# Performance work log

Measured on AMD Instinct MI355X. Metric: run time of the kernel, lower is better.

Reference implementation:

```python
import math
import jax, jax.numpy as jnp
import numpy as np

D_MODEL = 1024
NHEAD = 16
HEAD_DIM = D_MODEL // NHEAD
BATCH = 2
SEQ = 2048


def setup_inputs() -> dict:
    key = jax.random.key(0)
    ks = jax.random.split(key, 8)
    data = jax.random.normal(ks[0], (BATCH, SEQ, D_MODEL), dtype=jnp.float32)
    temporal = jax.random.uniform(ks[1], (BATCH, SEQ), dtype=jnp.float32)
    mask = jnp.zeros((SEQ, SEQ), dtype=jnp.float32)
    s = 1.0 / math.sqrt(D_MODEL)
    Wq = jax.random.normal(ks[2], (D_MODEL, D_MODEL), dtype=jnp.float32) * s
    Wk = jax.random.normal(ks[3], (D_MODEL, D_MODEL), dtype=jnp.float32) * s
    Wv = jax.random.normal(ks[4], (D_MODEL, D_MODEL), dtype=jnp.float32) * s
    bq = jax.random.normal(ks[5], (D_MODEL,), dtype=jnp.float32) * 0.02
    bk = jax.random.normal(ks[6], (D_MODEL,), dtype=jnp.float32) * 0.02
    bv = jax.random.normal(ks[7], (D_MODEL,), dtype=jnp.float32) * 0.02
    return {"data": data, "temporal": temporal, "mask": mask,
            "Wq": Wq, "bq": bq, "Wk": Wk, "bk": bk, "Wv": Wv, "bv": bv}


def _rotate_half_pairs(x):
    # x: [..., s] with s even; pairs (x0,x1) -> (-x1, x0) interleaved
    x2 = x.reshape(x.shape[:-1] + (-1, 2))  # [..., s//2, 2]
    rot = jnp.stack([-x2[..., 1], x2[..., 0]], axis=-1)
    return rot.reshape(x.shape)


def reference(data, temporal, mask, Wq, bq, Wk, bk, Wv, bv):
    B, L, D = data.shape
    H, S = NHEAD, HEAD_DIM
    scale = math.sqrt(S)

    query = (data @ Wq + bq).reshape(B, L, H, S)
    key_ = (data @ Wk + bk).reshape(B, L, H, S)
    value = (data @ Wv + bv).reshape(B, L, H, S)

    # freq = 10000^(-arange(0, S, 2)/S), repeat_interleave(2) -> [S]
    freq = jnp.power(10000.0, -jnp.arange(0, S, 2, dtype=jnp.float32) / S)
    freq = jnp.repeat(freq, 2)
    freqs = temporal[:, :, None] * freq[None, None, :]  # [B, L, S]
    cosine = jnp.cos(freqs)[:, :, None, :]  # [B, L, 1, S]
    sine = jnp.sin(freqs)[:, :, None, :]

    rq = query * cosine + _rotate_half_pairs(query) * sine
    rk = key_ * cosine + _rotate_half_pairs(key_) * sine

    logits = jnp.einsum('bqhs,bkhs->bhqk', rq, rk) / scale
    logits = logits + mask  # mask: [L, L], broadcasts over b,h
    weights = jax.nn.softmax(logits, axis=-1)
    context = jnp.einsum('bhqk,bkhs->bqhs', weights, value)
    return context.reshape(B, L, D)
```

## Files before the change

### kernel.cpp

```cpp
#include <hip/hip_runtime.h>
#include <hip/hip_bf16.h>

#define D_MODEL 1024
#define NHEAD   16
#define HEAD_DIM 64
#define BATCH   2
#define SEQ     2048
#define NTOK    (BATCH*SEQ)

#define FREQ_LOG2 0.20762050593046015f

typedef short  bfrag __attribute__((ext_vector_type(8)));
typedef float  ffrag __attribute__((ext_vector_type(4)));

__device__ inline ushort f2bf(float x) {
    __hip_bfloat16 h = __float2bfloat16(x);
    return __builtin_bit_cast(ushort, h);
}
__device__ inline float bf2f(ushort u) {
    return __builtin_bit_cast(float, (uint)u << 16);
}
__device__ inline void split_bf(float x, ushort& hi, ushort& lo) {
    __hip_bfloat16 h = __float2bfloat16(x);
    hi = __builtin_bit_cast(ushort, h);
    lo = f2bf(x - __bfloat162float(h));
}

__device__ inline void gload16(const ushort* g, ushort* l) {
    __builtin_amdgcn_global_load_lds(
        (const __attribute__((address_space(1))) void*)g,
        (__attribute__((address_space(3))) void*)l, 16, 0, 0);
}

__device__ inline void barrier_lds_only() {
    asm volatile("s_waitcnt lgkmcnt(0)\n\ts_barrier" ::: "memory");
}

__device__ inline void barrier_vm4() {
    asm volatile("s_waitcnt vmcnt(4) lgkmcnt(0)\n\ts_barrier" ::: "memory");
}

__device__ inline void barrier_vm8() {
    asm volatile("s_waitcnt vmcnt(8) lgkmcnt(0)\n\ts_barrier" ::: "memory");
}

__global__ __launch_bounds__(256)
void prep(const float* __restrict__ data, ushort* __restrict__ Ahi,
          ushort* __restrict__ Alo,
          const float* __restrict__ mask, ushort* __restrict__ Mbf,
          int* __restrict__ MZnz,
          const float* __restrict__ Wq, const float* __restrict__ Wk,
          const float* __restrict__ Wv, ushort* __restrict__ WThi,
          const float* __restrict__ temporal, float* __restrict__ cst)
{
    __shared__ float T[64][65];
    __shared__ int bnz;
    const int bid = blockIdx.x, t = threadIdx.x;

    if (bid < 4096) {
        const int i4 = (bid * 256 + t) * 4;
        const float4 v = *(const float4*)(data + i4);
        ushort4 h, l;
        split_bf(v.x, h.x, l.x); split_bf(v.y, h.y, l.y);
        split_bf(v.z, h.z, l.z); split_bf(v.w, h.w, l.w);
        *(ushort4*)(Ahi + i4) = h;
        *(ushort4*)(Alo + i4) = l;
        return;
    }
    if (bid < 8192) {
        const int mi = bid - 4096;
        const int i4 = (mi * 256 + t) * 4;
        const float4 v = *(const float4*)(mask + i4);
        ushort4 h;
        h.x = f2bf(v.x); h.y = f2bf(v.y); h.z = f2bf(v.z); h.w = f2bf(v.w);
        *(ushort4*)(Mbf + i4) = h;
        const int nz = (v.x != 0.f) || (v.y != 0.f) || (v.z != 0.f) || (v.w != 0.f);
        if (t == 0) bnz = 0;
        __syncthreads();
        if (nz) atomicOr(&bnz, 1);
        __syncthreads();
        if (t == 0) MZnz[mi] = bnz;
        return;
    }
    if (bid < 8960) {
        const int id  = bid - 8192;
        const int z   = id >> 8;
        const int rem = id & 255;
        const int k0  = (rem & 15) * 64, n0 = (rem >> 4) * 64;
        const float* W = (z == 0) ? Wq : (z == 1) ? Wk : Wv;
        ushort* thi = WThi + (size_t)z * D_MODEL * D_MODEL;

        #pragma unroll
        for (int i = 0; i < 4; i++) {
            const int f = i * 256 + t, r = f >> 4, c = (f & 15) * 4;
            const float4 v = *(const float4*)(W + (size_t)(k0 + r) * D_MODEL + n0 + c);
            T[r][c] = v.x; T[r][c + 1] = v.y; T[r][c + 2] = v.z; T[r][c + 3] = v.w;
        }
        __syncthreads();
        #pragma unroll
        for (int i = 0; i < 4; i++) {
            const int f = i * 256 + t, nr = f >> 4, kc = (f & 15) * 4;
            ushort4 h;
            h.x = f2bf(T[kc + 0][nr]);
            h.y = f2bf(T[kc + 1][nr]);
            h.z = f2bf(T[kc + 2][nr]);
            h.w = f2bf(T[kc + 3][nr]);
            const size_t o = (size_t)(n0 + nr) * D_MODEL + k0 + kc;
            *(ushort4*)(thi + o) = h;
        }
        return;
    }
    const int id3 = bid - 8960;
    const int m   = id3 * 8 + (t >> 5);
    const int j   = t & 31;
    const float tv = temporal[m];
    const float fr = exp2f(-(float)(2 * j) * FREQ_LOG2);
    float s, c;
    __sincosf(tv * fr, &s, &c);
    *(float2*)(cst + (size_t)m * 64 + 2 * j) = make_float2(c, s);
}

#define BK 32

union GemmSM {
    ushort st[3][2][128 * BK];
    float  c[64 * 132];
};

__global__ __launch_bounds__(256, 3)
void gemm_qkv(const ushort* __restrict__ Ahi, const ushort* __restrict__ Alo,
              const ushort* __restrict__ WThi,
              const float* __restrict__ bq, const float* __restrict__ bk,
              const float* __restrict__ bv, const float* __restrict__ cst,
              const int* __restrict__ MZnz, int* __restrict__ Flag,
              ushort* __restrict__ Qhi, ushort* __restrict__ Qlo,
              ushort* __restrict__ Khi,
              ushort* __restrict__ VT)
{
    __shared__ GemmSM sm;
    __shared__ int flg;
    const int bidl = blockIdx.x;
    const int xcd  = bidl & 7, kk = bidl >> 3;
    const int m0   = (xcd * 4 + (kk & 3)) * 128;
    const int nz   = kk >> 2;
    const int n0   = (nz & 7) * 128;
    const int z    = nz >> 3;

    const int t = threadIdx.x;

    if (bidl == 0) {
        if (t == 0) flg = 0;
        __syncthreads();
        int acc = 0;
        const int4* z4 = (const int4*)MZnz;
        #pragma unroll
        for (int i = 0; i < 4; i++) {
            const int4 v = z4[t * 4 + i];
            acc |= v.x | v.y | v.z | v.w;
        }
        if (acc) atomicOr(&flg, 1);
        __syncthreads();
        if (t == 0) Flag[0] = flg;
    }

    const float* bias = (z == 0) ? bq : (z == 1) ? bk : bv;
    const ushort* Bh = WThi + (size_t)z * D_MODEL * D_MODEL;

    const int w = t >> 6, lane = t & 63;
    const int lane15 = lane & 15, quad8 = (lane >> 4) * 8, quad = lane >> 4;
    const int wm = (w >> 1) * 64, wn = (w & 1) * 64;

    ffrag acc[4][4];
    #pragma unroll
    for (int i = 0; i < 4; i++)
        #pragma unroll
        for (int j = 0; j < 4; j++) acc[i][j] = (ffrag){0.f, 0.f, 0.f, 0.f};

    const int wr = w * 32;
    const int lr = lane >> 2;
    const int lc = (((lane & 3) ^ ((lane >> 3) & 3))) * 8;

    auto stage = [&](int bsel, int k0) {
        #pragma unroll
        for (int ch = 0; ch < 2; ch++) {
            const int rb = wr + ch * 16;
            const ushort* ga = Ahi + (size_t)(m0 + rb + lr) * D_MODEL + k0 + lc;
            const ushort* gb = Bh  + (size_t)(n0 + rb + lr) * D_MODEL + k0 + lc;
            gload16(ga, &sm.st[bsel][0][rb * BK]);
            gload16(gb, &sm.st[bsel][1][rb * BK]);
        }
    };

    bfrag alp0, alp1, alp2, alp3;
    {
        alp0 = *(const bfrag*)(Alo + (size_t)(m0 + wm +  0 + lane15) * D_MODEL + quad8);
        alp1 = *(const bfrag*)(Alo + (size_t)(m0 + wm + 16 + lane15) * D_MODEL + quad8);
        alp2 = *(const bfrag*)(Alo + (size_t)(m0 + wm + 32 + lane15) * D_MODEL + quad8);
        alp3 = *(const bfrag*)(Alo + (size_t)(m0 + wm + 48 + lane15) * D_MODEL + quad8);
    }

    stage(0, 0);
    stage(1, BK);
    barrier_vm4();

    const int rdsw = (quad ^ ((lane15 >> 1) & 3)) * 8;

    int cur = 0;
    for (int i = 0; i < 32; i++) {
        const int k0 = i * BK;
        const int st2 = (cur >= 1) ? cur - 1 : 2;
        stage(st2, k0 + 2 * BK);

        bfrag al0 = alp0, al1 = alp1, al2 = alp2, al3 = alp3;
        {
            const int kn = k0 + BK;
            alp0 = *(const bfrag*)(Alo + (size_t)(m0 + wm +  0 + lane15) * D_MODEL + kn + quad8);
            alp1 = *(const bfrag*)(Alo + (size_t)(m0 + wm + 16 + lane15) * D_MODEL + kn + quad8);
            alp2 = *(const bfrag*)(Alo + (size_t)(m0 + wm + 32 + lane15) * D_MODEL + kn + quad8);
            alp3 = *(const bfrag*)(Alo + (size_t)(m0 + wm + 48 + lane15) * D_MODEL + kn + quad8);
        }

        bfrag ah[4];
        #pragma unroll
        for (int mt = 0; mt < 4; mt++)
            ah[mt] = *(const bfrag*)&sm.st[cur][0][(wm + mt * 16 + lane15) * BK + rdsw];

        #pragma unroll
        for (int nt = 0; nt < 4; nt++) {
            const bfrag bh = *(const bfrag*)&sm.st[cur][1][(wn + nt * 16 + lane15) * BK + rdsw];
            {
                ffrag a = acc[0][nt];
                a = __builtin_amdgcn_mfma_f32_16x16x32_bf16(ah[0], bh, a, 0, 0, 0);
                a = __builtin_amdgcn_mfma_f32_16x16x32_bf16(al0,   bh, a, 0, 0, 0);
                acc[0][nt] = a;
            }
            {
                ffrag a = acc[1][nt];
                a = __builtin_amdgcn_mfma_f32_16x16x32_bf16(ah[1], bh, a, 0, 0, 0);
                a = __builtin_amdgcn_mfma_f32_16x16x32_bf16(al1,   bh, a, 0, 0, 0);
                acc[1][nt] = a;
            }
            {
                ffrag a = acc[2][nt];
                a = __builtin_amdgcn_mfma_f32_16x16x32_bf16(ah[2], bh, a, 0, 0, 0);
                a = __builtin_amdgcn_mfma_f32_16x16x32_bf16(al2,   bh, a, 0, 0, 0);
                acc[2][nt] = a;
            }
            {
                ffrag a = acc[3][nt];
                a = __builtin_amdgcn_mfma_f32_16x16x32_bf16(ah[3], bh, a, 0, 0, 0);
                a = __builtin_amdgcn_mfma_f32_16x16x32_bf16(al3,   bh, a, 0, 0, 0);
                acc[3][nt] = a;
            }
        }
        barrier_vm8();
        cur = (cur == 2) ? 0 : cur + 1;
    }

    float bn[4];
    #pragma unroll
    for (int nt = 0; nt < 4; nt++) bn[nt] = bias[n0 + wn + nt * 16 + lane15];

    const int CST = (z == 2) ? 129 : 132;

    #pragma unroll
    for (int p = 0; p < 2; p++) {
        if (p) __syncthreads();
        if ((w >> 1) == p) {
            #pragma unroll
            for (int mt = 0; mt < 4; mt++)
                #pragma unroll
                for (int nt = 0; nt < 4; nt++)
                    #pragma unroll
                    for (int rr = 0; rr < 4; rr++)
                        sm.c[(mt * 16 + quad * 4 + rr) * CST + wn + nt * 16 + lane15] =
                            acc[mt][nt][rr] + bn[nt];
        }
        __syncthreads();

        if (z < 2) {
            ushort* ohi = (z == 0) ? Qhi : Khi;
            const float sc = (z == 0) ? 0.125f : 1.0f;
            #pragma unroll
            for (int i = 0; i < 8; i++) {
                const int f = i * 256 + t, r = f >> 5, c4 = (f & 31) * 4;
                float4 v = *(float4*)&sm.c[r * 132 + c4];
                const int m = m0 + p * 64 + r;
                const float4 cs4 = *(const float4*)(cst + (size_t)m * 64 + (c4 & 63));
                const float c0 = cs4.x, s0 = cs4.y, c1v = cs4.z, s1 = cs4.w;
                const float y0 = (v.x * c0 - v.y * s0) * sc;
                const float y1 = (v.y * c0 + v.x * s0) * sc;
                const float y2 = (v.z * c1v - v.w * s1) * sc;
                const float y3 = (v.w * c1v + v.z * s1) * sc;
                ushort4 h, l;
                split_bf(y0, h.x, l.x); split_bf(y1, h.y, l.y);
                split_bf(y2, h.z, l.z); split_bf(y3, h.w, l.w);
                const size_t o = (size_t)m * D_MODEL + n0 + c4;
                *(ushort4*)(ohi + o) = h;
                if (z == 0) *(ushort4*)(Qlo + o) = l;
            }
        } else {
            const int bb = m0 >> 11;
            #pragma unroll
            for (int i = 0; i < 4; i++) {
                const int cid = i * 256 + t, col = cid >> 3, tg = (cid & 7) * 8;
                ushort u8[8];
                #pragma unroll
                for (int j = 0; j < 8; j++) u8[j] = f2bf(sm.c[(tg + j) * 129 + col]);
                const int ncol = n0 + col, hh = ncol >> 6, d = ncol & 63;
                const size_t dst = ((size_t)(bb * NHEAD + hh) * HEAD_DIM + d) * SEQ +
                                   (m0 & (SEQ - 1)) + p * 64 + tg;
                *(int4*)(VT + dst) = *(int4*)u8;
            }
        }
    }
}

__global__ __launch_bounds__(256, 2)
void attn_mfma(const ushort* __restrict__ Qhi, const ushort* __restrict__ Qlo,
               const ushort* __restrict__ Khi,
               const ushort* __restrict__ VT,  const ushort* __restrict__ maskbf,
               const int* __restrict__ Flag,
               float* __restrict__ out)
{
    __shared__ ushort lsK[2][128 * 64], lsV[2][64 * 128], lsP[128 * 64];

    const int bid  = blockIdx.x;
    const int bh   = (bid & 7) * 4 + (bid >> 7);
    const int qb   = (bid >> 3) & 15;
    const int b    = bh >> 4, h = bh & 15;
    const int q0   = qb * 128;

    const int t = threadIdx.x, w = t >> 6, lane = t & 63;
    const int lane15 = lane & 15, quad = lane >> 4;
    const size_t tok0 = (size_t)b * SEQ;

    const int mz = Flag[0];

    bfrag qh[2][2], ql[2][2];
    #pragma unroll
    for (int su = 0; su < 2; su++) {
        const size_t qrow = (tok0 + q0 + w * 32 + su * 16 + lane15) * D_MODEL +
                            h * HEAD_DIM;
        #pragma unroll
        for (int ks = 0; ks < 2; ks++) {
            qh[su][ks] = *(const bfrag*)(Qhi + qrow + ks * 32 + quad * 8);
            ql[su][ks] = *(const bfrag*)(Qlo + qrow + ks * 32 + quad * 8);
        }
    }

    const short one_bf = (short)0x3F80;
    const bfrag ones = {one_bf, one_bf, one_bf, one_bf,
                        one_bf, one_bf, one_bf, one_bf};

    ffrag of[2][4], of_l[2];
    #pragma unroll
    for (int su = 0; su < 2; su++) {
        of_l[su] = (ffrag){0.f, 0.f, 0.f, 0.f};
        #pragma unroll
        for (int nt = 0; nt < 4; nt++)
            of[su][nt] = (ffrag){0.f, 0.f, 0.f, 0.f};
    }

    const int rK  = t >> 3, cK = (t & 7) * 8;
    const int swK = ((t & 7) ^ (rK & 7)) * 8;
    const int rV   = t >> 2;
    const int keyV = ((rV & 3) << 2) | ((rV >> 2) & 3);
    const ushort* Kh0 = Khi + tok0 * D_MODEL + h * HEAD_DIM;
    const ushort* Vt0 = VT + (size_t)(b * NHEAD + h) * HEAD_DIM * SEQ;

    const size_t kof0 = (size_t)(rK +  0) * D_MODEL + cK;
    const size_t kof1 = (size_t)(rK + 32) * D_MODEL + cK;
    const size_t kof2 = (size_t)(rK + 64) * D_MODEL + cK;
    const size_t kof3 = (size_t)(rK + 96) * D_MODEL + cK;
    const size_t vof  = (size_t)rV * SEQ + (t & 3) * 8;

    int4 pk0 = *(const int4*)(Kh0 + kof0);
    int4 pk1 = *(const int4*)(Kh0 + kof1);
    int4 pk2 = *(const int4*)(Kh0 + kof2);
    int4 pk3 = *(const int4*)(Kh0 + kof3);
    int4 pv0 = *(const int4*)(Vt0 + vof +  0);
    int4 pv1 = *(const int4*)(Vt0 + vof + 32);
    int4 pv2 = *(const int4*)(Vt0 + vof + 64);
    int4 pv3 = *(const int4*)(Vt0 + vof + 96);

    *(int4*)&lsK[0][(rK +  0) * 64 + swK] = pk0;
    *(int4*)&lsK[0][(rK + 32) * 64 + swK] = pk1;
    *(int4*)&lsK[0][(rK + 64) * 64 + swK] = pk2;
    *(int4*)&lsK[0][(rK + 96) * 64 + swK] = pk3;
    *(int4*)&lsV[0][rV * 128 + (((t & 3) +  0) ^ keyV) * 8] = pv0;
    *(int4*)&lsV[0][rV * 128 + (((t & 3) +  4) ^ keyV) * 8] = pv1;
    *(int4*)&lsV[0][rV * 128 + (((t & 3) +  8) ^ keyV) * 8] = pv2;
    *(int4*)&lsV[0][rV * 128 + (((t & 3) + 12) ^ keyV) * 8] = pv3;

    pk0 = *(const int4*)(Kh0 + 128 * D_MODEL + kof0);
    pk1 = *(const int4*)(Kh0 + 128 * D_MODEL + kof1);
    pk2 = *(const int4*)(Kh0 + 128 * D_MODEL + kof2);
    pk3 = *(const int4*)(Kh0 + 128 * D_MODEL + kof3);
    pv0 = *(const int4*)(Vt0 + 128 + vof +  0);
    pv1 = *(const int4*)(Vt0 + 128 + vof + 32);
    pv2 = *(const int4*)(Vt0 + 128 + vof + 64);
    pv3 = *(const int4*)(Vt0 + 128 + vof + 96);
    barrier_lds_only();

    const ushort* mrow0 = maskbf + (size_t)(q0 + w * 32 + quad * 4) * SEQ;
    const ushort* mrow1 = maskbf + (size_t)(q0 + w * 32 + 16 + quad * 4) * SEQ;

    const int krd  = lane15 & 7;
    const int keyr = (((lane15 >> 2) & 3) << 1) | (lane15 & 1);
    const int keyVr = ((lane15 & 3) << 2) | ((lane15 >> 2) & 3);

    int cur = 0;
    for (int kt = 0; kt < SEQ; kt += 128) {
        if (kt + 128 < SEQ) {
            *(int4*)&lsK[cur ^ 1][(rK +  0) * 64 + swK] = pk0;
            *(int4*)&lsK[cur ^ 1][(rK + 32) * 64 + swK] = pk1;
            *(int4*)&lsK[cur ^ 1][(rK + 64) * 64 + swK] = pk2;
            *(int4*)&lsK[cur ^ 1][(rK + 96) * 64 + swK] = pk3;
            *(int4*)&lsV[cur ^ 1][rV * 128 + (((t & 3) +  0) ^ keyV) * 8] = pv0;
            *(int4*)&lsV[cur ^ 1][rV * 128 + (((t & 3) +  4) ^ keyV) * 8] = pv1;
            *(int4*)&lsV[cur ^ 1][rV * 128 + (((t & 3) +  8) ^ keyV) * 8] = pv2;
            *(int4*)&lsV[cur ^ 1][rV * 128 + (((t & 3) + 12) ^ keyV) * 8] = pv3;
        }

        const int ktn = (kt + 256 < SEQ) ? kt + 256 : 0;
        const ushort* KhT = Kh0 + (size_t)ktn * D_MODEL;
        const ushort* VtT = Vt0 + ktn;
        pk0 = *(const int4*)(KhT + kof0);
        pk1 = *(const int4*)(KhT + kof1);
        pk2 = *(const int4*)(KhT + kof2);
        pk3 = *(const int4*)(KhT + kof3);
        pv0 = *(const int4*)(VtT + vof +  0);
        pv1 = *(const int4*)(VtT + vof + 32);
        pv2 = *(const int4*)(VtT + vof + 64);
        pv3 = *(const int4*)(VtT + vof + 96);

        #pragma unroll
        for (int half = 0; half < 2; half++) {
            const int kb = kt + half * 64;

            float mv0[4][4], mv1[4][4];
            if (mz) {
                #pragma unroll
                for (int nt = 0; nt < 4; nt++)
                    #pragma unroll
                    for (int rr = 0; rr < 4; rr++) {
                        mv0[nt][rr] = bf2f(mrow0[(size_t)rr * SEQ + kb + nt * 16 + lane15]);
                        mv1[nt][rr] = bf2f(mrow1[(size_t)rr * SEQ + kb + nt * 16 + lane15]);
                    }
            }

            ffrag s0[4], s1[4];
            __builtin_amdgcn_s_setprio(1);
            #pragma unroll
            for (int nt = 0; nt < 4; nt++) {
                const int krow = half * 64 + nt * 16 + lane15;
                const bfrag kf0 = *(const bfrag*)&lsK[cur][krow * 64 + ((0 + quad) ^ krd) * 8];
                const bfrag kf1 = *(const bfrag*)&lsK[cur][krow * 64 + ((4 + quad) ^ krd) * 8];
                ffrag a0 = (ffrag){0.f, 0.f, 0.f, 0.f};
                ffrag a1 = (ffrag){0.f, 0.f, 0.f, 0.f};
                a0 = __builtin_amdgcn_mfma_f32_16x16x32_bf16(qh[0][0], kf0, a0, 0, 0, 0);
                a0 = __builtin_amdgcn_mfma_f32_16x16x32_bf16(ql[0][0], kf0, a0, 0, 0, 0);
                a0 = __builtin_amdgcn_mfma_f32_16x16x32_bf16(qh[0][1], kf1, a0, 0, 0, 0);
                a0 = __builtin_amdgcn_mfma_f32_16x16x32_bf16(ql[0][1], kf1, a0, 0, 0, 0);
                a1 = __builtin_amdgcn_mfma_f32_16x16x32_bf16(qh[1][0], kf0, a1, 0, 0, 0);
                a1 = __builtin_amdgcn_mfma_f32_16x16x32_bf16(ql[1][0], kf0, a1, 0, 0, 0);
                a1 = __builtin_amdgcn_mfma_f32_16x16x32_bf16(qh[1][1], kf1, a1, 0, 0, 0);
                a1 = __builtin_amdgcn_mfma_f32_16x16x32_bf16(ql[1][1], kf1, a1, 0, 0, 0);
                s0[nt] = a0;
                s1[nt] = a1;
            }
            __builtin_amdgcn_s_setprio(0);

            #pragma unroll
            for (int nt = 0; nt < 4; nt++)
                #pragma unroll
                for (int rr = 0; rr < 4; rr++) {
                    const int pchk = (2 * nt + (lane15 >> 3)) ^ ((quad << 1) | (rr & 1));
                    float x0 = s0[nt][rr];
                    float x1 = s1[nt][rr];
                    if (mz) { x0 += mv0[nt][rr]; x1 += mv1[nt][rr]; }
                    const float e0 = __expf(x0);
                    lsP[(w * 32 + quad * 4 + rr) * 64 + pchk * 8 + (lane15 & 7)] = f2bf(e0);
                    const float e1 = __expf(x1);
                    lsP[(w * 32 + 16 + quad * 4 + rr) * 64 + pchk * 8 + (lane15 & 7)] = f2bf(e1);
                }

            __builtin_amdgcn_s_setprio(1);
            #pragma unroll
            for (int ksl = 0; ksl < 2; ksl++) {
                const bfrag pf0 = *(const bfrag*)&lsP[(w * 32 + lane15) * 64 +
                                                      ((ksl * 4 + quad) ^ keyr) * 8];
                const bfrag pf1 = *(const bfrag*)&lsP[(w * 32 + 16 + lane15) * 64 +
                                                      ((ksl * 4 + quad) ^ keyr) * 8];
                const int lkc = half * 8 + ksl * 4 + quad;
                #pragma unroll
                for (int nt = 0; nt < 4; nt++) {
                    const bfrag vf = *(const bfrag*)&lsV[cur][(nt * 16 + lane15) * 128 +
                                                              (lkc ^ keyVr) * 8];
                    of[0][nt] = __builtin_amdgcn_mfma_f32_16x16x32_bf16(pf0, vf, of[0][nt], 0, 0, 0);
                    of[1][nt] = __builtin_amdgcn_mfma_f32_16x16x32_bf16(pf1, vf, of[1][nt], 0, 0, 0);
                }
                of_l[0] = __builtin_amdgcn_mfma_f32_16x16x32_bf16(pf0, ones, of_l[0], 0, 0, 0);
                of_l[1] = __builtin_amdgcn_mfma_f32_16x16x32_bf16(pf1, ones, of_l[1], 0, 0, 0);
            }
            __builtin_amdgcn_s_setprio(0);
        }

        barrier_lds_only();
        cur ^= 1;
    }

    #pragma unroll
    for (int su = 0; su < 2; su++) {
        float inv[4];
        #pragma unroll
        for (int rr = 0; rr < 4; rr++)
            inv[rr] = 1.0f / of_l[su][rr];
        #pragma unroll
        for (int nt = 0; nt < 4; nt++)
            #pragma unroll
            for (int rr = 0; rr < 4; rr++)
                out[(tok0 + q0 + w * 32 + su * 16 + quad * 4 + rr) * D_MODEL +
                    h * HEAD_DIM + nt * 16 + lane15] = of[su][nt][rr] * inv[rr];
    }
}

extern "C" void kernel_launch(void* const* d_in, const int* in_sizes, int n_in,
                              void* d_out, int out_size, void* d_ws, size_t ws_size,
                              hipStream_t stream)
{
    const float* data     = (const float*)d_in[0];
    const float* temporal = (const float*)d_in[1];
    const float* mask     = (const float*)d_in[2];
    const float* Wq = (const float*)d_in[3];
    const float* bq = (const float*)d_in[4];
    const float* Wk = (const float*)d_in[5];
    const float* bk = (const float*)d_in[6];
    const float* Wv = (const float*)d_in[7];
    const float* bv = (const float*)d_in[8];
    float* out = (float*)d_out;

    char* ws = (char*)d_ws;
    const size_t MB = 1024 * 1024;
    ushort* Ahi  = (ushort*)(ws + 0 * MB);
    ushort* Alo  = (ushort*)(ws + 8 * MB);
    ushort* WThi = (ushort*)(ws + 16 * MB);
    int*    MZnz = (int*)   (ws + 22 * MB);
    int*    Flag = (int*)   (ws + 23 * MB);
    float*  cst  = (float*) (ws + 24 * MB);
    ushort* Qhi  = (ushort*)(ws + 28 * MB);
    ushort* Qlo  = (ushort*)(ws + 36 * MB);
    ushort* Khi  = (ushort*)(ws + 44 * MB);
    ushort* VT   = (ushort*)(ws + 60 * MB);
    ushort* Mbf  = (ushort*)(ws + 68 * MB);

    prep<<<dim3(9472), 256, 0, stream>>>(data, Ahi, Alo, mask, Mbf, MZnz,
                                         Wq, Wk, Wv, WThi, temporal, cst);
    gemm_qkv<<<dim3(768), 256, 0, stream>>>(
        Ahi, Alo, WThi, bq, bk, bv, cst, MZnz, Flag,
        Qhi, Qlo, Khi, VT);
    attn_mfma<<<dim3(BATCH * NHEAD * SEQ / 128), 256, 0, stream>>>(
        Qhi, Qlo, Khi, VT, Mbf, Flag, out);
}
```

Baseline: 235.6 us.

## Run QKV GEMM with 512 threads per block and smaller per-wave tiles

The QKV projection GEMM now launches 512 threads (8 waves) per 128x128 tile instead of 256, so each wave owns a 32x64 sub-tile instead of 64x64. Staging is spread over all threads with one load per operand per thread, and the wait counts and epilogue loops are adjusted to match. The aim is more waves in flight to hide memory latency and cut accumulator register pressure. In exchange each wave reads more shared memory per MFMA, and scheduling overhead grows.

```diff
diff --git a/kernel.cpp b/kernel.cpp
--- a/kernel.cpp
+++ b/kernel.cpp
@@ -36,12 +36,12 @@
     asm volatile("s_waitcnt lgkmcnt(0)\n\ts_barrier" ::: "memory");
 }
 
+__device__ inline void barrier_vm2() {
+    asm volatile("s_waitcnt vmcnt(2) lgkmcnt(0)\n\ts_barrier" ::: "memory");
+}
+
 __device__ inline void barrier_vm4() {
     asm volatile("s_waitcnt vmcnt(4) lgkmcnt(0)\n\ts_barrier" ::: "memory");
-}
-
-__device__ inline void barrier_vm8() {
-    asm volatile("s_waitcnt vmcnt(8) lgkmcnt(0)\n\ts_barrier" ::: "memory");
 }
 
 __global__ __launch_bounds__(256)
@@ -127,7 +127,7 @@
     float  c[64 * 132];
 };
 
-__global__ __launch_bounds__(256, 3)
+__global__ __launch_bounds__(512, 6)
 void gemm_qkv(const ushort* __restrict__ Ahi, const ushort* __restrict__ Alo,
               const ushort* __restrict__ WThi,
               const float* __restrict__ bq, const float* __restrict__ bk,
@@ -151,14 +151,16 @@
     if (bidl == 0) {
         if (t == 0) flg = 0;
         __syncthreads();
-        int acc = 0;
-        const int4* z4 = (const int4*)MZnz;
-        #pragma unroll
-        for (int i = 0; i < 4; i++) {
-            const int4 v = z4[t * 4 + i];
-            acc |= v.x | v.y | v.z | v.w;
-        }
-        if (acc) atomicOr(&flg, 1);
+        if (t < 256) {
+            int acc = 0;
+            const int4* z4 = (const int4*)MZnz;
+            #pragma unroll
+            for (int i = 0; i < 4; i++) {
+                const int4 v = z4[t * 4 + i];
+                acc |= v.x | v.y | v.z | v.w;
+            }
+            if (acc) atomicOr(&flg, 1);
+        }
         __syncthreads();
         if (t == 0) Flag[0] = flg;
     }
@@ -167,41 +169,35 @@
     const ushort* Bh = WThi + (size_t)z * D_MODEL * D_MODEL;
 
     const int w = t >> 6, lane = t & 63;
-    const int lane15 = lane & 15, quad8 = (lane >> 4) * 8, quad = lane >> 4;
-    const int wm = (w >> 1) * 64, wn = (w & 1) * 64;
-
-    ffrag acc[4][4];
+    const int lane15 = lane & 15, quad = lane >> 4;
+    const int wm = (w & 3) * 32;
+    const int wn = (w >> 2) * 64;
+
+    ffrag acc[2][4];
     #pragma unroll
-    for (int i = 0; i < 4; i++)
+    for (int i = 0; i < 2; i++)
         #pragma unroll
         for (int j = 0; j < 4; j++) acc[i][j] = (ffrag){0.f, 0.f, 0.f, 0.f};
 
-    const int wr = w * 32;
-    const int lr = lane >> 2;
-    const int lc = (((lane & 3) ^ ((lane >> 3) & 3))) * 8;
+    const int sr = t >> 2;
+    const int lc = (((t & 3) ^ ((t >> 3) & 3))) * 8;
+    const int wbase = (t >> 6) * 16 * BK;
 
     auto stage = [&](int bsel, int k0) {
-        #pragma unroll
-        for (int ch = 0; ch < 2; ch++) {
-            const int rb = wr + ch * 16;
-            const ushort* ga = Ahi + (size_t)(m0 + rb + lr) * D_MODEL + k0 + lc;
-            const ushort* gb = Bh  + (size_t)(n0 + rb + lr) * D_MODEL + k0 + lc;
-            gload16(ga, &sm.st[bsel][0][rb * BK]);
-            gload16(gb, &sm.st[bsel][1][rb * BK]);
-        }
+        const ushort* ga = Ahi + (size_t)(m0 + sr) * D_MODEL + k0 + lc;
+        const ushort* gb = Bh  + (size_t)(n0 + sr) * D_MODEL + k0 + lc;
+        gload16(ga, &sm.st[bsel][0][wbase]);
+        gload16(gb, &sm.st[bsel][1][wbase]);
     };
 
-    bfrag alp0, alp1, alp2, alp3;
-    {
-        alp0 = *(const bfrag*)(Alo + (size_t)(m0 + wm +  0 + lane15) * D_MODEL + quad8);
-        alp1 = *(const bfrag*)(Alo + (size_t)(m0 + wm + 16 + lane15) * D_MODEL + quad8);
-        alp2 = *(const bfrag*)(Alo + (size_t)(m0 + wm + 32 + lane15) * D_MODEL + quad8);
-        alp3 = *(const bfrag*)(Alo + (size_t)(m0 + wm + 48 + lane15) * D_MODEL + quad8);
-    }
+    const int quad8 = quad * 8;
+    bfrag alp0, alp1;
+    alp0 = *(const bfrag*)(Alo + (size_t)(m0 + wm +  0 + lane15) * D_MODEL + quad8);
+    alp1 = *(const bfrag*)(Alo + (size_t)(m0 + wm + 16 + lane15) * D_MODEL + quad8);
 
     stage(0, 0);
     stage(1, BK);
-    barrier_vm4();
+    barrier_vm2();
 
     const int rdsw = (quad ^ ((lane15 >> 1) & 3)) * 8;
 
@@ -211,49 +207,33 @@
         const int st2 = (cur >= 1) ? cur - 1 : 2;
         stage(st2, k0 + 2 * BK);
 
-        bfrag al0 = alp0, al1 = alp1, al2 = alp2, al3 = alp3;
+        bfrag al0 = alp0, al1 = alp1;
         {
             const int kn = k0 + BK;
             alp0 = *(const bfrag*)(Alo + (size_t)(m0 + wm +  0 + lane15) * D_MODEL + kn + quad8);
             alp1 = *(const bfrag*)(Alo + (size_t)(m0 + wm + 16 + lane15) * D_MODEL + kn + quad8);
-            alp2 = *(const bfrag*)(Alo + (size_t)(m0 + wm + 32 + lane15) * D_MODEL + kn + quad8);
-            alp3 = *(const bfrag*)(Alo + (size_t)(m0 + wm + 48 + lane15) * D_MODEL + kn + quad8);
-        }
-
-        bfrag ah[4];
-        #pragma unroll
-        for (int mt = 0; mt < 4; mt++)
-            ah[mt] = *(const bfrag*)&sm.st[cur][0][(wm + mt * 16 + lane15) * BK + rdsw];
+        }
+
+        bfrag ah0 = *(const bfrag*)&sm.st[cur][0][(wm +  0 + lane15) * BK + rdsw];
+        bfrag ah1 = *(const bfrag*)&sm.st[cur][0][(wm + 16 + lane15) * BK + rdsw];
 
         #pragma unroll
         for (int nt = 0; nt < 4; nt++) {
             const bfrag bh = *(const bfrag*)&sm.st[cur][1][(wn + nt * 16 + lane15) * BK + rdsw];
             {
                 ffrag a = acc[0][nt];
-                a = __builtin_amdgcn_mfma_f32_16x16x32_bf16(ah[0], bh, a, 0, 0, 0);
-                a = __builtin_amdgcn_mfma_f32_16x16x32_bf16(al0,   bh, a, 0, 0, 0);
+                a = __builtin_amdgcn_mfma_f32_16x16x32_bf16(ah0, bh, a, 0, 0, 0);
+                a = __builtin_amdgcn_mfma_f32_16x16x32_bf16(al0, bh, a, 0, 0, 0);
                 acc[0][nt] = a;
             }
             {
                 ffrag a = acc[1][nt];
-                a = __builtin_amdgcn_mfma_f32_16x16x32_bf16(ah[1], bh, a, 0, 0, 0);
-                a = __builtin_amdgcn_mfma_f32_16x16x32_bf16(al1,   bh, a, 0, 0, 0);
+                a = __builtin_amdgcn_mfma_f32_16x16x32_bf16(ah1, bh, a, 0, 0, 0);
+                a = __builtin_amdgcn_mfma_f32_16x16x32_bf16(al1, bh, a, 0, 0, 0);
                 acc[1][nt] = a;
             }
-            {
-                ffrag a = acc[2][nt];
-                a = __builtin_amdgcn_mfma_f32_16x16x32_bf16(ah[2], bh, a, 0, 0, 0);
-                a = __builtin_amdgcn_mfma_f32_16x16x32_bf16(al2,   bh, a, 0, 0, 0);
-                acc[2][nt] = a;
-            }
-            {
-                ffrag a = acc[3][nt];
-                a = __builtin_amdgcn_mfma_f32_16x16x32_bf16(ah[3], bh, a, 0, 0, 0);
-                a = __builtin_amdgcn_mfma_f32_16x16x32_bf16(al3,   bh, a, 0, 0, 0);
-                acc[3][nt] = a;
-            }
-        }
-        barrier_vm8();
+        }
+        barrier_vm4();
         cur = (cur == 2) ? 0 : cur + 1;
     }
 
@@ -262,19 +242,20 @@
     for (int nt = 0; nt < 4; nt++) bn[nt] = bias[n0 + wn + nt * 16 + lane15];
 
     const int CST = (z == 2) ? 129 : 132;
+    const int wlow = w & 1;
 
     #pragma unroll
     for (int p = 0; p < 2; p++) {
         if (p) __syncthreads();
-        if ((w >> 1) == p) {
-            #pragma unroll
-            for (int mt = 0; mt < 4; mt++)
+        if (((w & 3) >> 1) == p) {
+            #pragma unroll
+            for (int mt = 0; mt < 2; mt++)
                 #pragma unroll
                 for (int nt = 0; nt < 4; nt++)
                     #pragma unroll
                     for (int rr = 0; rr < 4; rr++)
-                        sm.c[(mt * 16 + quad * 4 + rr) * CST + wn + nt * 16 + lane15] =
-                            acc[mt][nt][rr] + bn[nt];
+                        sm.c[(wlow * 32 + mt * 16 + quad * 4 + rr) * CST +
+                             wn + nt * 16 + lane15] = acc[mt][nt][rr] + bn[nt];
         }
         __syncthreads();
 
@@ -282,8 +263,8 @@
             ushort* ohi = (z == 0) ? Qhi : Khi;
             const float sc = (z == 0) ? 0.125f : 1.0f;
             #pragma unroll
-            for (int i = 0; i < 8; i++) {
-                const int f = i * 256 + t, r = f >> 5, c4 = (f & 31) * 4;
+            for (int i = 0; i < 4; i++) {
+                const int f = i * 512 + t, r = f >> 5, c4 = (f & 31) * 4;
                 float4 v = *(float4*)&sm.c[r * 132 + c4];
                 const int m = m0 + p * 64 + r;
                 const float4 cs4 = *(const float4*)(cst + (size_t)m * 64 + (c4 & 63));
@@ -302,8 +283,8 @@
         } else {
             const int bb = m0 >> 11;
             #pragma unroll
-            for (int i = 0; i < 4; i++) {
-                const int cid = i * 256 + t, col = cid >> 3, tg = (cid & 7) * 8;
+            for (int i = 0; i < 2; i++) {
+                const int cid = i * 512 + t, col = cid >> 3, tg = (cid & 7) * 8;
                 ushort u8[8];
                 #pragma unroll
                 for (int j = 0; j < 8; j++) u8[j] = f2bf(sm.c[(tg + j) * 129 + col]);
@@ -557,7 +538,7 @@
 
     prep<<<dim3(9472), 256, 0, stream>>>(data, Ahi, Alo, mask, Mbf, MZnz,
                                          Wq, Wk, Wv, WThi, temporal, cst);
-    gemm_qkv<<<dim3(768), 256, 0, stream>>>(
+    gemm_qkv<<<dim3(768), 512, 0, stream>>>(
         Ahi, Alo, WThi, bq, bk, bv, cst, MZnz, Flag,
         Qhi, Qlo, Khi, VT);
     attn_mfma<<<dim3(BATCH * NHEAD * SEQ / 128), 256, 0, stream>>>(
```

New measurement: 263.4 us. 11.8% more time.
